# Kernel tuning notes

Hardware: AMD Instinct MI355X
Metric: run time of the kernel (lower is better)

Reference implementation:

```python
import jax, jax.numpy as jnp
import numpy as np

B, S, H, I, E, TOP_K = 2, 2048, 1024, 2048, 8, 2


def setup_inputs() -> dict:
    key = jax.random.key(0)
    k1, k2, k3, k4, k5 = jax.random.split(key, 5)
    scale_h = 1.0 / np.sqrt(H)
    scale_i = 1.0 / np.sqrt(I)
    return {
        "hidden_states": jax.random.normal(k1, (B, S, H), dtype=jnp.float32),
        "router_w": jax.random.normal(k2, (H, E), dtype=jnp.float32) * scale_h,
        "gate_w": jax.random.normal(k3, (E, H, I), dtype=jnp.float32) * scale_h,
        "up_w": jax.random.normal(k4, (E, H, I), dtype=jnp.float32) * scale_h,
        "out_w": jax.random.normal(k5, (E, I, H), dtype=jnp.float32) * scale_i,
    }


def reference(hidden_states, router_w, gate_w, up_w, out_w):
    b, s, h = hidden_states.shape
    x = hidden_states.reshape(-1, h)  # [T, H], T = B*S

    # Router: logits -> softmax -> top-k -> renormalize -> dense routing matrix
    router_logits = x @ router_w  # [T, E]
    router_probs = jax.nn.softmax(router_logits, axis=-1)
    top_p, top_i = jax.lax.top_k(router_probs, TOP_K)  # [T, K]
    top_p = top_p / jnp.sum(top_p, axis=-1, keepdims=True)
    one_hot = jax.nn.one_hot(top_i, E, dtype=top_p.dtype)  # [T, K, E]
    routing_full = jnp.sum(one_hot * top_p[..., None], axis=1)  # [T, E]
    routing_full = routing_full.T  # [E, T]

    # Dense all-expert FFN (SwiGLU), as in the original batched einsum form
    gate = jnp.einsum("th,ehm->etm", x, gate_w)  # [E, T, I]
    gate = jax.nn.silu(gate)
    intermediate = jnp.einsum("th,ehm->etm", x, up_w)  # [E, T, I]
    hidden = intermediate * gate
    expert_out = jnp.einsum("eti,eih->eth", hidden, out_w)  # [E, T, H]

    # Weighted combine over experts
    out = jnp.sum(expert_out * routing_full[:, :, None], axis=0)  # [T, H]
    out = out.reshape(b, s, h)
    return out, router_logits
```

## Files before the change

kernel.cpp:

```cpp
#include <hip/hip_runtime.h>
#include <hip/hip_bf16.h>
#include <stdint.h>

#define TT 4096
#define HH 1024
#define II 2048
#define EE 8
#define RB 64
#define CSTRIDE 32

typedef short bf16x8 __attribute__((ext_vector_type(8)));
typedef float f32x4 __attribute__((ext_vector_type(4)));

__device__ __forceinline__ unsigned short f2bf(float f) {
  unsigned u = __float_as_uint(f);
  u += 0x7FFF + ((u >> 16) & 1);
  return (unsigned short)(u >> 16);
}

__device__ __forceinline__ void gl_lds16(const void* g, void* l) {
  auto gp = reinterpret_cast<const __attribute__((address_space(1))) unsigned int*>(
      reinterpret_cast<uintptr_t>(g));
  auto lp = reinterpret_cast<__attribute__((address_space(3))) unsigned int*>(
      reinterpret_cast<uintptr_t>(l));
  __builtin_amdgcn_global_load_lds(gp, lp, 16, 0, 0);
}

__global__ void prep_kernel(const float* __restrict__ gw, const float* __restrict__ uw,
                            const float* __restrict__ ow, const float* __restrict__ x,
                            unsigned short* __restrict__ gwt, unsigned short* __restrict__ uwt,
                            unsigned short* __restrict__ owt, unsigned short* __restrict__ xb) {
  __shared__ unsigned int tl[64 * 32];
  int z = blockIdx.z;
  int which = z >> 3, e = z & 7;
  int tid = threadIdx.x;

  if (which == 3) {
    size_t b0 = (size_t)blockIdx.x * 8192;
#pragma unroll
    for (int it = 0; it < 4; ++it) {
      size_t i = b0 + it * 2048 + tid * 8;
      float4 a = *(const float4*)(x + i);
      float4 b = *(const float4*)(x + i + 4);
      union { unsigned short s[8]; uint4 v; } o;
      o.s[0] = f2bf(a.x); o.s[1] = f2bf(a.y); o.s[2] = f2bf(a.z); o.s[3] = f2bf(a.w);
      o.s[4] = f2bf(b.x); o.s[5] = f2bf(b.y); o.s[6] = f2bf(b.z); o.s[7] = f2bf(b.w);
      *(uint4*)(xb + i) = o.v;
    }
    return;
  }

  const float* in; unsigned short* out; int M, N;
  if (which == 0)      { in = gw; out = gwt; M = HH; N = II; }
  else if (which == 1) { in = uw; out = uwt; M = HH; N = II; }
  else                 { in = ow; out = owt; M = II; N = HH; }
  int nb = N / 64;
  int bx = blockIdx.x % nb, by = blockIdx.x / nb;
  size_t base = (size_t)e * M * N;
  int mB = by * 64, nB = bx * 64;

  union F4 { float4 v; float f[4]; };
  int c4 = (tid & 15) * 4;
  int mp = tid >> 4;
#pragma unroll
  for (int it = 0; it < 2; ++it) {
    int m = (mp + it * 16) * 2;
    const float* p0 = in + base + (size_t)(mB + m) * N + nB + c4;
    F4 a, b;
    a.v = *(const float4*)p0;
    b.v = *(const float4*)(p0 + N);
    int mdw = m >> 1;
#pragma unroll
    for (int i = 0; i < 4; ++i) {
      int n = c4 + i;
      unsigned v = (unsigned)f2bf(a.f[i]) | ((unsigned)f2bf(b.f[i]) << 16);
      tl[n * 32 + ((mdw + n) & 31)] = v;
    }
  }
  __syncthreads();
  int n2 = tid >> 3;
  int md8 = (tid & 7) * 4;
#pragma unroll
  for (int it = 0; it < 2; ++it) {
    int n = n2 + it * 32;
    unsigned vv[4];
#pragma unroll
    for (int i = 0; i < 4; ++i)
      vv[i] = tl[n * 32 + ((md8 + i + n) & 31)];
    uint4 o4 = make_uint4(vv[0], vv[1], vv[2], vv[3]);
    *(uint4*)(out + base + (size_t)(nB + n) * M + mB + md8 * 2) = o4;
  }
}

__global__ void router_kernel(const float* __restrict__ x, const float* __restrict__ rw,
                              float* __restrict__ logits_out, int* __restrict__ cnt,
                              int* __restrict__ list, int* __restrict__ tslot,
                              float2* __restrict__ tw) {
  __shared__ int bcnt[EE];
  __shared__ int bbase[EE];
  __shared__ int te[RB][2];
  int tid = threadIdx.x, wave = tid >> 6, lane = tid & 63;
  if (tid < EE) bcnt[tid] = 0;
  __syncthreads();
  int t0 = blockIdx.x * RB;

  for (int sub = 0; sub < RB / 4; ++sub) {
    int li = sub * 4 + wave;
    int t = t0 + li;
    float acc[EE];
#pragma unroll
    for (int e = 0; e < EE; ++e) acc[e] = 0.f;
#pragma unroll
    for (int j = 0; j < 4; ++j) {
      int h = j * 256 + lane * 4;
      union F4 { float4 v; float f[4]; } xv;
      xv.v = *(const float4*)(x + (size_t)t * HH + h);
#pragma unroll
      for (int i = 0; i < 4; ++i) {
        const float4* r4 = (const float4*)(rw + (h + i) * EE);
        float4 r0 = r4[0], r1 = r4[1];
        float xs = xv.f[i];
        acc[0] += xs * r0.x; acc[1] += xs * r0.y; acc[2] += xs * r0.z; acc[3] += xs * r0.w;
        acc[4] += xs * r1.x; acc[5] += xs * r1.y; acc[6] += xs * r1.z; acc[7] += xs * r1.w;
      }
    }
#pragma unroll
    for (int e = 0; e < EE; ++e)
#pragma unroll
      for (int off = 32; off; off >>= 1) acc[e] += __shfl_down(acc[e], off);
    if (lane == 0) {
      float4* lo = (float4*)(logits_out + (size_t)t * EE);
      lo[0] = make_float4(acc[0], acc[1], acc[2], acc[3]);
      lo[1] = make_float4(acc[4], acc[5], acc[6], acc[7]);
      int e0 = 0; float b0 = acc[0];
#pragma unroll
      for (int e = 1; e < EE; ++e) if (acc[e] > b0) { b0 = acc[e]; e0 = e; }
      int e1 = -1; float b1 = -3.4e38f;
#pragma unroll
      for (int e = 0; e < EE; ++e) if (e != e0 && acc[e] > b1) { b1 = acc[e]; e1 = e; }
      float w0 = 1.f / (1.f + __expf(b1 - b0));
      tw[t] = make_float2(w0, 1.f - w0);
      int lp0 = atomicAdd(&bcnt[e0], 1);
      int lp1 = atomicAdd(&bcnt[e1], 1);
      te[li][0] = e0 | (lp0 << 8);
      te[li][1] = e1 | (lp1 << 8);
    }
  }
  __syncthreads();
  if (tid < EE) bbase[tid] = atomicAdd(&cnt[tid * CSTRIDE], bcnt[tid]);
  __syncthreads();
  if (tid < RB * 2) {
    int li = tid >> 1, s = tid & 1;
    int v = te[li][s];
    int e = v & 255, lp = v >> 8;
    int p = bbase[e] + lp;
    int t = t0 + li;
    list[e * TT + p] = t;
    tslot[t * 2 + s] = (e << 16) | p;
  }
}

__launch_bounds__(256, 3)
__global__ void gemm1_kernel(const unsigned short* __restrict__ xb,
                             const unsigned short* __restrict__ gwt,
                             const unsigned short* __restrict__ uwt,
                             unsigned short* __restrict__ hidden,
                             const int* __restrict__ cnt, const int* __restrict__ list) {
  int e = blockIdx.z;
  int cn = cnt[e * CSTRIDE];
  int hb0 = 0;
  for (int i = 0; i < EE; ++i) hb0 += (i < e) ? cnt[i * CSTRIDE] : 0;
  int mBase = blockIdx.y * 128;
  if (mBase >= cn) return;
  int nBase = blockIdx.x * 64;

  __shared__ __align__(16) unsigned short smem[16384];
  __shared__ int stok[128];

  int tid = threadIdx.x, wave = tid >> 6, lane = tid & 63;
  if (tid < 128) {
    int g = mBase + tid;
    stok[tid] = list[e * TT + (g < cn ? g : cn - 1)];
  }
  __syncthreads();

  const char* gaddr[8];
#pragma unroll
  for (int j = 0; j < 8; ++j) {
    int c = wave * 512 + j * 64 + lane;
    const char* g;
    if (c < 1024) {
      int r = c >> 3, sl = (c & 7) ^ (r & 7);
      g = (const char*)xb + (size_t)stok[r] * (HH * 2) + sl * 16;
    } else if (c < 1536) {
      int cc = c - 1024, r = cc >> 3, sl = (cc & 7) ^ (r & 7);
      g = (const char*)gwt + ((size_t)e * II + nBase + r) * (HH * 2) + sl * 16;
    } else {
      int cc = c - 1536, r = cc >> 3, sl = (cc & 7) ^ (r & 7);
      g = (const char*)uwt + ((size_t)e * II + nBase + r) * (HH * 2) + sl * 16;
    }
    gaddr[j] = g;
  }

  int q = lane >> 4, m16 = lane & 15;
  int wr = wave & 1, wc = wave >> 1;
  int faddrA[4][2], faddrBg[2][2], faddrBu[2][2];
#pragma unroll
  for (int mi = 0; mi < 4; ++mi) {
    int R = wr * 64 + mi * 16 + m16;
#pragma unroll
    for (int h = 0; h < 2; ++h)
      faddrA[mi][h] = (R * 8 + ((h * 4 + q) ^ (R & 7))) * 16;
  }
#pragma unroll
  for (int ni = 0; ni < 2; ++ni) {
    int n = wc * 32 + ni * 16 + m16;
#pragma unroll
    for (int h = 0; h < 2; ++h) {
      faddrBg[ni][h] = (1024 + n * 8 + ((h * 4 + q) ^ (n & 7))) * 16;
      faddrBu[ni][h] = (1536 + n * 8 + ((h * 4 + q) ^ (n & 7))) * 16;
    }
  }

  f32x4 zero4 = {0.f, 0.f, 0.f, 0.f};
  f32x4 accG[4][2], accU[4][2];
#pragma unroll
  for (int mi = 0; mi < 4; ++mi)
#pragma unroll
    for (int ni = 0; ni < 2; ++ni) { accG[mi][ni] = zero4; accU[mi][ni] = zero4; }

  const char* smemc = (const char*)smem;
  for (int kt = 0; kt < HH / 64; ++kt) {
    __syncthreads();
#pragma unroll
    for (int j = 0; j < 8; ++j) {
      gl_lds16(gaddr[j], (char*)smem + (size_t)(wave * 512 + j * 64) * 16);
      gaddr[j] += 128;
    }
    __syncthreads();
#pragma unroll
    for (int h = 0; h < 2; ++h) {
      bf16x8 aF[4], bG[2], bU[2];
#pragma unroll
      for (int mi = 0; mi < 4; ++mi) aF[mi] = *(const bf16x8*)(smemc + faddrA[mi][h]);
#pragma unroll
      for (int ni = 0; ni < 2; ++ni) {
        bG[ni] = *(const bf16x8*)(smemc + faddrBg[ni][h]);
        bU[ni] = *(const bf16x8*)(smemc + faddrBu[ni][h]);
      }
#pragma unroll
      for (int mi = 0; mi < 4; ++mi)
#pragma unroll
        for (int ni = 0; ni < 2; ++ni) {
          accG[mi][ni] = __builtin_amdgcn_mfma_f32_16x16x32_bf16(aF[mi], bG[ni], accG[mi][ni], 0, 0, 0);
          accU[mi][ni] = __builtin_amdgcn_mfma_f32_16x16x32_bf16(aF[mi], bU[ni], accU[mi][ni], 0, 0, 0);
        }
    }
  }

  int hb = hb0 + mBase;
  int rowsValid = cn - mBase; if (rowsValid > 128) rowsValid = 128;
#pragma unroll
  for (int mi = 0; mi < 4; ++mi)
#pragma unroll
    for (int ni = 0; ni < 2; ++ni)
#pragma unroll
      for (int r = 0; r < 4; ++r) {
        int row = wr * 64 + mi * 16 + q * 4 + r;
        if (row < rowsValid) {
          float g = accG[mi][ni][r], u = accU[mi][ni][r];
          float h = g / (1.f + __expf(-g)) * u;
          hidden[(size_t)(hb + row) * II + nBase + wc * 32 + ni * 16 + m16] = f2bf(h);
        }
      }
}

__launch_bounds__(256, 3)
__global__ void gemm2_kernel(const unsigned short* __restrict__ hidden,
                             const unsigned short* __restrict__ owt,
                             float* __restrict__ expert_out,
                             const int* __restrict__ cnt) {
  int e = blockIdx.z;
  int cn = cnt[e * CSTRIDE];
  int hb0 = 0;
  for (int i = 0; i < EE; ++i) hb0 += (i < e) ? cnt[i * CSTRIDE] : 0;
  int mBase = blockIdx.y * 128;
  if (mBase >= cn) return;
  int nBase = blockIdx.x * 64;

  __shared__ __align__(16) unsigned short smem[12288];

  int tid = threadIdx.x, wave = tid >> 6, lane = tid & 63;
  int hb = hb0 + mBase;
  const char* gaddr[6];
#pragma unroll
  for (int j = 0; j < 6; ++j) {
    int c = wave * 384 + j * 64 + lane;
    const char* g;
    if (c < 1024) {
      int r = c >> 3, sl = (c & 7) ^ (r & 7);
      g = (const char*)hidden + (size_t)(hb + r) * (II * 2) + sl * 16;
    } else {
      int cc = c - 1024, r = cc >> 3, sl = (cc & 7) ^ (r & 7);
      g = (const char*)owt + ((size_t)e * HH + nBase + r) * (II * 2) + sl * 16;
    }
    gaddr[j] = g;
  }

  int q = lane >> 4, m16 = lane & 15;
  int wr = wave & 1, wc = wave >> 1;
  int faddrA[4][2], faddrB[2][2];
#pragma unroll
  for (int mi = 0; mi < 4; ++mi) {
    int R = wr * 64 + mi * 16 + m16;
#pragma unroll
    for (int h = 0; h < 2; ++h)
      faddrA[mi][h] = (R * 8 + ((h * 4 + q) ^ (R & 7))) * 16;
  }
#pragma unroll
  for (int ni = 0; ni < 2; ++ni) {
    int n = wc * 32 + ni * 16 + m16;
#pragma unroll
    for (int h = 0; h < 2; ++h)
      faddrB[ni][h] = (1024 + n * 8 + ((h * 4 + q) ^ (n & 7))) * 16;
  }

  f32x4 zero4 = {0.f, 0.f, 0.f, 0.f};
  f32x4 acc[4][2];
#pragma unroll
  for (int mi = 0; mi < 4; ++mi)
#pragma unroll
    for (int ni = 0; ni < 2; ++ni) acc[mi][ni] = zero4;

  const char* smemc = (const char*)smem;
  for (int kt = 0; kt < II / 64; ++kt) {
    __syncthreads();
#pragma unroll
    for (int j = 0; j < 6; ++j) {
      gl_lds16(gaddr[j], (char*)smem + (size_t)(wave * 384 + j * 64) * 16);
      gaddr[j] += 128;
    }
    __syncthreads();
#pragma unroll
    for (int h = 0; h < 2; ++h) {
      bf16x8 aF[4], bF[2];
#pragma unroll
      for (int mi = 0; mi < 4; ++mi) aF[mi] = *(const bf16x8*)(smemc + faddrA[mi][h]);
#pragma unroll
      for (int ni = 0; ni < 2; ++ni) bF[ni] = *(const bf16x8*)(smemc + faddrB[ni][h]);
#pragma unroll
      for (int mi = 0; mi < 4; ++mi)
#pragma unroll
        for (int ni = 0; ni < 2; ++ni)
          acc[mi][ni] = __builtin_amdgcn_mfma_f32_16x16x32_bf16(aF[mi], bF[ni], acc[mi][ni], 0, 0, 0);
    }
  }

  int rowsValid = cn - mBase; if (rowsValid > 128) rowsValid = 128;
#pragma unroll
  for (int mi = 0; mi < 4; ++mi)
#pragma unroll
    for (int ni = 0; ni < 2; ++ni)
#pragma unroll
      for (int r = 0; r < 4; ++r) {
        int row = wr * 64 + mi * 16 + q * 4 + r;
        if (row < rowsValid)
          expert_out[(size_t)(hb + row) * HH + nBase + wc * 32 + ni * 16 + m16] = acc[mi][ni][r];
      }
}

__global__ void combine_kernel(const float* __restrict__ expert_out,
                               const int* __restrict__ cnt, const int* __restrict__ tslot,
                               const float2* __restrict__ tw, float* __restrict__ out) {
  int pre[EE];
  int s = 0;
#pragma unroll
  for (int e = 0; e < EE; ++e) { pre[e] = s; s += cnt[e * CSTRIDE]; }
  int t = blockIdx.x;
  int s0 = tslot[t * 2], s1 = tslot[t * 2 + 1];
  float2 w = tw[t];
  int r0 = pre[s0 >> 16] + (s0 & 0xFFFF);
  int r1 = pre[s1 >> 16] + (s1 & 0xFFFF);
  const float4* a = (const float4*)(expert_out + (size_t)r0 * HH);
  const float4* b = (const float4*)(expert_out + (size_t)r1 * HH);
  float4* o = (float4*)(out + (size_t)t * HH);
  int c = threadIdx.x;
  float4 av = a[c], bv = b[c];
  o[c] = make_float4(w.x * av.x + w.y * bv.x, w.x * av.y + w.y * bv.y,
                     w.x * av.z + w.y * bv.z, w.x * av.w + w.y * bv.w);
}

extern "C" void kernel_launch(void* const* d_in, const int* in_sizes, int n_in,
                              void* d_out, int out_size, void* d_ws, size_t ws_size,
                              hipStream_t stream) {
  (void)in_sizes; (void)n_in; (void)out_size; (void)ws_size;
  const float* x  = (const float*)d_in[0];
  const float* rw = (const float*)d_in[1];
  const float* gw = (const float*)d_in[2];
  const float* uw = (const float*)d_in[3];
  const float* ow = (const float*)d_in[4];
  float* out = (float*)d_out;
  float* logits = out + (size_t)TT * HH;

  char* ws = (char*)d_ws;
  size_t o = 0;
  auto alloc = [&](size_t bytes) {
    char* p = ws + o;
    o += (bytes + 255) & ~(size_t)255;
    return p;
  };
  unsigned short* xb  = (unsigned short*)alloc((size_t)TT * HH * 2);
  unsigned short* gwt = (unsigned short*)alloc((size_t)EE * II * HH * 2);
  unsigned short* uwt = (unsigned short*)alloc((size_t)EE * II * HH * 2);
  unsigned short* owt = (unsigned short*)alloc((size_t)EE * HH * II * 2);
  unsigned short* hidden = (unsigned short*)alloc((size_t)(2 * TT + 128) * II * 2);
  int*   cnt   = (int*)alloc(EE * CSTRIDE * 4);
  int*   list  = (int*)alloc((size_t)EE * TT * 4);
  int*   tslot = (int*)alloc((size_t)TT * 2 * 4);
  float2* tw   = (float2*)alloc((size_t)TT * 8);
  float* expert_out = (float*)gwt;

  hipMemsetAsync(cnt, 0, EE * CSTRIDE * 4, stream);

  prep_kernel<<<dim3(512, 1, 4 * EE), 256, 0, stream>>>(gw, uw, ow, x, gwt, uwt, owt, xb);
  router_kernel<<<TT / RB, 256, 0, stream>>>(x, rw, logits, cnt, list, tslot, tw);
  gemm1_kernel<<<dim3(II / 64, TT / 128, EE), 256, 0, stream>>>(xb, gwt, uwt, hidden, cnt, list);
  gemm2_kernel<<<dim3(HH / 64, TT / 128, EE), 256, 0, stream>>>(hidden, owt, expert_out, cnt);
  combine_kernel<<<TT, 256, 0, stream>>>(expert_out, cnt, tslot, tw, out);
}
```

Measured before the change: 462.3 us.

## Fuse weight prep into router and gemm1 launches, replace atomics with deterministic scan scatter

Removes the standalone prep kernel. The gate/up weight transposes and the bf16 conversion of x now run in the same launch as the router, and the out-weight transpose runs as extra blocks inside the gemm1 grid. Router blocks shrink to 16 tokens and write per-block expert counts; a new scatter kernel prefix-sums them and builds the expert lists, which replaces the global atomics and the memset. This removes a launch and lets the transpose work overlap with routing and GEMM work. The cost is an extra small kernel, and every scatter block redundantly scans all 256 blocks' counts.

Result: faster. 403.1 us (-12.8%).

```diff
diff --git a/kernel.cpp b/kernel.cpp
--- a/kernel.cpp
+++ b/kernel.cpp
@@ -6,7 +6,8 @@
 #define HH 1024
 #define II 2048
 #define EE 8
-#define RB 64
+#define RB 16
+#define NRB (TT / RB)
 #define CSTRIDE 32
 
 typedef short bf16x8 __attribute__((ext_vector_type(8)));
@@ -26,46 +27,17 @@
   __builtin_amdgcn_global_load_lds(gp, lp, 16, 0, 0);
 }
 
-__global__ void prep_kernel(const float* __restrict__ gw, const float* __restrict__ uw,
-                            const float* __restrict__ ow, const float* __restrict__ x,
-                            unsigned short* __restrict__ gwt, unsigned short* __restrict__ uwt,
-                            unsigned short* __restrict__ owt, unsigned short* __restrict__ xb) {
-  __shared__ unsigned int tl[64 * 32];
-  int z = blockIdx.z;
-  int which = z >> 3, e = z & 7;
-  int tid = threadIdx.x;
-
-  if (which == 3) {
-    size_t b0 = (size_t)blockIdx.x * 8192;
-#pragma unroll
-    for (int it = 0; it < 4; ++it) {
-      size_t i = b0 + it * 2048 + tid * 8;
-      float4 a = *(const float4*)(x + i);
-      float4 b = *(const float4*)(x + i + 4);
-      union { unsigned short s[8]; uint4 v; } o;
-      o.s[0] = f2bf(a.x); o.s[1] = f2bf(a.y); o.s[2] = f2bf(a.z); o.s[3] = f2bf(a.w);
-      o.s[4] = f2bf(b.x); o.s[5] = f2bf(b.y); o.s[6] = f2bf(b.z); o.s[7] = f2bf(b.w);
-      *(uint4*)(xb + i) = o.v;
-    }
-    return;
-  }
-
-  const float* in; unsigned short* out; int M, N;
-  if (which == 0)      { in = gw; out = gwt; M = HH; N = II; }
-  else if (which == 1) { in = uw; out = uwt; M = HH; N = II; }
-  else                 { in = ow; out = owt; M = II; N = HH; }
-  int nb = N / 64;
-  int bx = blockIdx.x % nb, by = blockIdx.x / nb;
-  size_t base = (size_t)e * M * N;
-  int mB = by * 64, nB = bx * 64;
-
+__device__ __forceinline__ void transpose_tile(const float* __restrict__ in,
+                                               unsigned short* __restrict__ out,
+                                               int M, int N, int mB, int nB,
+                                               unsigned int* tl, int tid) {
   union F4 { float4 v; float f[4]; };
   int c4 = (tid & 15) * 4;
   int mp = tid >> 4;
 #pragma unroll
   for (int it = 0; it < 2; ++it) {
     int m = (mp + it * 16) * 2;
-    const float* p0 = in + base + (size_t)(mB + m) * N + nB + c4;
+    const float* p0 = in + (size_t)(mB + m) * N + nB + c4;
     F4 a, b;
     a.v = *(const float4*)p0;
     b.v = *(const float4*)(p0 + N);
@@ -88,21 +60,37 @@
     for (int i = 0; i < 4; ++i)
       vv[i] = tl[n * 32 + ((md8 + i + n) & 31)];
     uint4 o4 = make_uint4(vv[0], vv[1], vv[2], vv[3]);
-    *(uint4*)(out + base + (size_t)(nB + n) * M + mB + md8 * 2) = o4;
-  }
-}
-
-__global__ void router_kernel(const float* __restrict__ x, const float* __restrict__ rw,
-                              float* __restrict__ logits_out, int* __restrict__ cnt,
-                              int* __restrict__ list, int* __restrict__ tslot,
-                              float2* __restrict__ tw) {
+    *(uint4*)(out + (size_t)(nB + n) * M + mB + md8 * 2) = o4;
+  }
+}
+
+__global__ void front_kernel(const float* __restrict__ x, const float* __restrict__ rw,
+                             const float* __restrict__ gw, const float* __restrict__ uw,
+                             float* __restrict__ logits_out, unsigned short* __restrict__ xb,
+                             unsigned short* __restrict__ gwt, unsigned short* __restrict__ uwt,
+                             int* __restrict__ gcnt, int2* __restrict__ ttop) {
+  __shared__ unsigned int tl[2048];
+  int b = blockIdx.x;
+  int tid = threadIdx.x;
+
+  if (b >= NRB) {
+    int idx = b - NRB;
+    int which = idx >> 12;
+    int r = idx & 4095;
+    int e = r >> 9;
+    int tile = r & 511;
+    int bx = tile & 31, by = tile >> 5;
+    const float* in = (which ? uw : gw) + (size_t)e * HH * II;
+    unsigned short* out = (which ? uwt : gwt) + (size_t)e * HH * II;
+    transpose_tile(in, out, HH, II, by * 64, bx * 64, tl, tid);
+    return;
+  }
+
   __shared__ int bcnt[EE];
-  __shared__ int bbase[EE];
-  __shared__ int te[RB][2];
-  int tid = threadIdx.x, wave = tid >> 6, lane = tid & 63;
+  int wave = tid >> 6, lane = tid & 63;
   if (tid < EE) bcnt[tid] = 0;
   __syncthreads();
-  int t0 = blockIdx.x * RB;
+  int t0 = b * RB;
 
   for (int sub = 0; sub < RB / 4; ++sub) {
     int li = sub * 4 + wave;
@@ -115,6 +103,10 @@
       int h = j * 256 + lane * 4;
       union F4 { float4 v; float f[4]; } xv;
       xv.v = *(const float4*)(x + (size_t)t * HH + h);
+      union { unsigned short s[4]; uint2 v; } pk;
+#pragma unroll
+      for (int i = 0; i < 4; ++i) pk.s[i] = f2bf(xv.f[i]);
+      *(uint2*)(xb + (size_t)t * HH + h) = pk.v;
 #pragma unroll
       for (int i = 0; i < 4; ++i) {
         const float4* r4 = (const float4*)(rw + (h + i) * EE);
@@ -139,34 +131,64 @@
 #pragma unroll
       for (int e = 0; e < EE; ++e) if (e != e0 && acc[e] > b1) { b1 = acc[e]; e1 = e; }
       float w0 = 1.f / (1.f + __expf(b1 - b0));
-      tw[t] = make_float2(w0, 1.f - w0);
       int lp0 = atomicAdd(&bcnt[e0], 1);
       int lp1 = atomicAdd(&bcnt[e1], 1);
-      te[li][0] = e0 | (lp0 << 8);
-      te[li][1] = e1 | (lp1 << 8);
-    }
-  }
-  __syncthreads();
-  if (tid < EE) bbase[tid] = atomicAdd(&cnt[tid * CSTRIDE], bcnt[tid]);
-  __syncthreads();
-  if (tid < RB * 2) {
-    int li = tid >> 1, s = tid & 1;
-    int v = te[li][s];
-    int e = v & 255, lp = v >> 8;
-    int p = bbase[e] + lp;
-    int t = t0 + li;
-    list[e * TT + p] = t;
-    tslot[t * 2 + s] = (e << 16) | p;
-  }
+      ttop[t] = make_int2(e0 | (e1 << 3) | (lp0 << 6) | (lp1 << 11), __float_as_int(w0));
+    }
+  }
+  __syncthreads();
+  if (tid < EE) gcnt[b * EE + tid] = bcnt[tid];
+}
+
+__global__ void scatter_kernel(const int* __restrict__ gcnt, const int2* __restrict__ ttop,
+                               int* __restrict__ cnt, int* __restrict__ list,
+                               int* __restrict__ tslot, float2* __restrict__ tw) {
+  __shared__ int raw[NRB * EE];
+  __shared__ int base[NRB][EE];
+  int tid = threadIdx.x;
+  for (int i = tid; i < NRB * EE; i += 256) raw[i] = gcnt[i];
+  __syncthreads();
+  if (tid < EE) {
+    int s = 0;
+    for (int b = 0; b < NRB; ++b) { base[b][tid] = s; s += raw[b * EE + tid]; }
+    if (blockIdx.x == 0) cnt[tid * CSTRIDE] = s;
+  }
+  __syncthreads();
+  int t = blockIdx.x * 256 + tid;
+  int2 ti = ttop[t];
+  int v = ti.x;
+  float w0 = __int_as_float(ti.y);
+  int e0 = v & 7, e1 = (v >> 3) & 7, lp0 = (v >> 6) & 31, lp1 = (v >> 11) & 31;
+  int b = t >> 4;
+  int p0 = base[b][e0] + lp0;
+  int p1 = base[b][e1] + lp1;
+  list[e0 * TT + p0] = t;
+  list[e1 * TT + p1] = t;
+  tslot[t * 2]     = (e0 << 16) | p0;
+  tslot[t * 2 + 1] = (e1 << 16) | p1;
+  tw[t] = make_float2(w0, 1.f - w0);
 }
 
 __launch_bounds__(256, 3)
 __global__ void gemm1_kernel(const unsigned short* __restrict__ xb,
                              const unsigned short* __restrict__ gwt,
                              const unsigned short* __restrict__ uwt,
+                             const float* __restrict__ ow, unsigned short* __restrict__ owt,
                              unsigned short* __restrict__ hidden,
                              const int* __restrict__ cnt, const int* __restrict__ list) {
+  __shared__ __align__(16) unsigned short smem[16384];
+  __shared__ int stok[128];
+  int tid = threadIdx.x;
   int e = blockIdx.z;
+
+  if (blockIdx.y >= 32) {
+    int tile = (blockIdx.y - 32) * 32 + blockIdx.x;
+    int bx = tile & 15, by = tile >> 4;
+    transpose_tile(ow + (size_t)e * II * HH, owt + (size_t)e * II * HH,
+                   II, HH, by * 64, bx * 64, (unsigned int*)smem, tid);
+    return;
+  }
+
   int cn = cnt[e * CSTRIDE];
   int hb0 = 0;
   for (int i = 0; i < EE; ++i) hb0 += (i < e) ? cnt[i * CSTRIDE] : 0;
@@ -174,10 +196,7 @@
   if (mBase >= cn) return;
   int nBase = blockIdx.x * 64;
 
-  __shared__ __align__(16) unsigned short smem[16384];
-  __shared__ int stok[128];
-
-  int tid = threadIdx.x, wave = tid >> 6, lane = tid & 63;
+  int wave = tid >> 6, lane = tid & 63;
   if (tid < 128) {
     int g = mBase + tid;
     stok[tid] = list[e * TT + (g < cn ? g : cn - 1)];
@@ -414,17 +433,17 @@
   unsigned short* uwt = (unsigned short*)alloc((size_t)EE * II * HH * 2);
   unsigned short* owt = (unsigned short*)alloc((size_t)EE * HH * II * 2);
   unsigned short* hidden = (unsigned short*)alloc((size_t)(2 * TT + 128) * II * 2);
-  int*   cnt   = (int*)alloc(EE * CSTRIDE * 4);
-  int*   list  = (int*)alloc((size_t)EE * TT * 4);
-  int*   tslot = (int*)alloc((size_t)TT * 2 * 4);
-  float2* tw   = (float2*)alloc((size_t)TT * 8);
+  int*    cnt   = (int*)alloc(EE * CSTRIDE * 4);
+  int*    list  = (int*)alloc((size_t)EE * TT * 4);
+  int*    tslot = (int*)alloc((size_t)TT * 2 * 4);
+  float2* tw    = (float2*)alloc((size_t)TT * 8);
+  int*    gcnt  = (int*)alloc((size_t)NRB * EE * 4);
+  int2*   ttop  = (int2*)alloc((size_t)TT * 8);
   float* expert_out = (float*)gwt;
 
-  hipMemsetAsync(cnt, 0, EE * CSTRIDE * 4, stream);
-
-  prep_kernel<<<dim3(512, 1, 4 * EE), 256, 0, stream>>>(gw, uw, ow, x, gwt, uwt, owt, xb);
-  router_kernel<<<TT / RB, 256, 0, stream>>>(x, rw, logits, cnt, list, tslot, tw);
-  gemm1_kernel<<<dim3(II / 64, TT / 128, EE), 256, 0, stream>>>(xb, gwt, uwt, hidden, cnt, list);
+  front_kernel<<<NRB + 8192, 256, 0, stream>>>(x, rw, gw, uw, logits, xb, gwt, uwt, gcnt, ttop);
+  scatter_kernel<<<TT / 256, 256, 0, stream>>>(gcnt, ttop, cnt, list, tslot, tw);
+  gemm1_kernel<<<dim3(32, 48, EE), 256, 0, stream>>>(xb, gwt, uwt, ow, owt, hidden, cnt, list);
   gemm2_kernel<<<dim3(HH / 64, TT / 128, EE), 256, 0, stream>>>(hidden, owt, expert_out, cnt);
   combine_kernel<<<TT, 256, 0, stream>>>(expert_out, cnt, tslot, tw, out);
 }
```
